# Performance work log

Hardware: AMD Instinct MI355X
Metric: run time of the kernel (lower is better)

Reference implementation:

```python
import jax, jax.numpy as jnp
import numpy as np
import math

FEAT_DIM = 128
N_BANK = 1000000
K_NEG = 4096
BATCH = 256
T = 0.5
MOMENTUM = 0.5
EPS = 1e-7


def setup_inputs() -> dict:
    key = jax.random.key(0)
    k1, k2, k3, k4, k5, k6 = jax.random.split(key, 6)
    stdv = 1.0 / math.sqrt(FEAT_DIM / 3)
    memory_l = jax.random.uniform(k1, (N_BANK, FEAT_DIM), minval=-stdv, maxval=stdv, dtype=jnp.float32)
    memory_ab = jax.random.uniform(k2, (N_BANK, FEAT_DIM), minval=-stdv, maxval=stdv, dtype=jnp.float32)
    l = jax.random.normal(k3, (BATCH, FEAT_DIM), dtype=jnp.float32)
    ab = jax.random.normal(k4, (BATCH, FEAT_DIM), dtype=jnp.float32)
    y = jax.random.randint(k5, (BATCH,), 0, N_BANK, dtype=jnp.int32)
    idx = jax.random.randint(k6, (BATCH, K_NEG + 1), 0, N_BANK, dtype=jnp.int32)
    idx = idx.at[:, 0].set(y)  # positive sample in slot 0, as in torch forward
    return {"l": l, "ab": ab, "memory_l": memory_l, "memory_ab": memory_ab, "y": y, "idx": idx}


def _l2_normalize(x):
    # matches torch: x / (sqrt(sum(x^2)) + eps)
    return x / (jnp.sqrt(jnp.sum(x * x, axis=1, keepdims=True)) + EPS)


def _momentum_update(memory, y, x_norm):
    # gather rows, momentum mix, renormalize, scatter back
    pos = memory[y] * MOMENTUM + x_norm * (1.0 - MOMENTUM)          # [B, D]
    norm = jnp.sqrt(jnp.sum(pos * pos, axis=1, keepdims=True))
    return memory.at[y].set(pos / norm)


def reference(l, ab, memory_l, memory_ab, y, idx):
    outputSize = memory_l.shape[0]
    ln = _l2_normalize(l)
    abn = _l2_normalize(ab)

    # gather negatives+positive from the AB bank, score against l features
    w_ab = jax.lax.stop_gradient(memory_ab[idx])                     # [B, K+1, D]
    P_l = jnp.exp(jnp.einsum('bkd,bd->bk', w_ab, ln) / T)[..., None]  # [B, K+1, 1]
    Z_l = jnp.mean(P_l) * outputSize
    out_l = P_l / Z_l

    w_l = jax.lax.stop_gradient(memory_l[idx])                       # [B, K+1, D]
    P_ab = jnp.exp(jnp.einsum('bkd,bd->bk', w_l, abn) / T)[..., None]
    Z_ab = jnp.mean(P_ab) * outputSize
    out_ab = P_ab / Z_ab

    # momentum scatter update of the memory banks (no_grad in torch)
    new_memory_l = jax.lax.stop_gradient(_momentum_update(memory_l, y, ln))
    new_memory_ab = jax.lax.stop_gradient(_momentum_update(memory_ab, y, abn))

    return out_l, out_ab, new_memory_l, new_memory_ab
```

## Files before the change

### kernel.cpp

```cpp
#include <hip/hip_runtime.h>
#include <math.h>
#include <stdint.h>

#define FEAT   128
#define NBANK  1000000
#define KP1    4097
#define BATCH  256
#define INV_T  2.0f
#define EPS_N  1e-7f

constexpr size_t TOTP   = (size_t)BATCH * KP1;
constexpr size_t O_OUTL = 0;
constexpr size_t O_OUTA = TOTP;
constexpr size_t O_MEML = 2 * TOTP;
constexpr size_t O_MEMA = O_MEML + (size_t)NBANK * FEAT;

constexpr int RPB   = 32;
constexpr int NBUCK = NBANK / RPB;

constexpr size_t WS_LN   = 0;
constexpr size_t WS_ABN  = 32768;
constexpr size_t WS_INVZ = 65536;
constexpr size_t WS_PL   = 65544;
constexpr size_t WS_PA   = 65800;
constexpr size_t WS_U32  = 66560;

typedef float vfloat4 __attribute__((ext_vector_type(4)));

__device__ __forceinline__ void nt_store4(vfloat4* p, vfloat4 v) {
    __builtin_nontemporal_store(v, p);
}
__device__ __forceinline__ float dot4(vfloat4 a, vfloat4 b) {
    return a.x * b.x + a.y * b.y + a.z * b.z + a.w * b.w;
}

__global__ void norm_kernel(const float* __restrict__ l,
                            const float* __restrict__ ab,
                            float* __restrict__ ws) {
    int b    = blockIdx.x;
    int lane = threadIdx.x;
    const float* src;
    float*       dst;
    if (b < BATCH) { src = l  + (size_t)b * FEAT;            dst = ws + WS_LN  + (size_t)b * FEAT; }
    else           { src = ab + (size_t)(b - BATCH) * FEAT;  dst = ws + WS_ABN + (size_t)(b - BATCH) * FEAT; }
    float2 v = *(const float2*)(src + 2 * lane);
    float  ss = v.x * v.x + v.y * v.y;
    #pragma unroll
    for (int m = 1; m < 64; m <<= 1) ss += __shfl_xor(ss, m, 64);
    float inv = 1.0f / (sqrtf(ss) + EPS_N);
    ((float2*)dst)[lane] = make_float2(v.x * inv, v.y * inv);
}

__global__ void zero_kernel(unsigned int* __restrict__ cnt) {
    int stride = gridDim.x * blockDim.x;
    for (int i = blockIdx.x * blockDim.x + threadIdx.x; i < NBUCK; i += stride)
        cnt[i] = 0u;
}

__global__ void hist_kernel(const int* __restrict__ idx,
                            unsigned int* __restrict__ cnt) {
    int stride = gridDim.x * blockDim.x;
    for (size_t p = (size_t)blockIdx.x * blockDim.x + threadIdx.x; p < TOTP; p += stride) {
        int row = idx[p];
        atomicAdd(&cnt[row >> 5], 1u);
    }
}

__global__ void scan_kernel(const unsigned int* __restrict__ cnt,
                            unsigned int* __restrict__ start,
                            unsigned int* __restrict__ cur) {
    __shared__ unsigned int ts[256];
    __shared__ unsigned int ex[256];
    int t = threadIdx.x;
    const int Q = (NBUCK + 255) / 256;
    int lo = t * Q, hi = lo + Q; if (hi > NBUCK) hi = NBUCK;
    unsigned int s = 0;
    for (int i = lo; i < hi; ++i) s += cnt[i];
    ts[t] = s;
    __syncthreads();
    if (t == 0) {
        unsigned int r = 0;
        for (int i = 0; i < 256; ++i) { ex[i] = r; r += ts[i]; }
    }
    __syncthreads();
    unsigned int base = ex[t];
    for (int i = lo; i < hi; ++i) {
        start[i] = base; cur[i] = base;
        base += cnt[i];
    }
}

__global__ void scatter_kernel(const int* __restrict__ idx,
                               unsigned int* __restrict__ cur,
                               unsigned int* __restrict__ ent) {
    int stride = gridDim.x * blockDim.x;
    for (size_t p = (size_t)blockIdx.x * blockDim.x + threadIdx.x; p < TOTP; p += stride) {
        int row = idx[p];
        int b   = (int)(p / KP1);
        int k   = (int)(p - (size_t)b * KP1);
        unsigned int pos = atomicAdd(&cur[row >> 5], 1u);
        ent[pos] = ((unsigned int)b << 18) | ((unsigned int)k << 5) | (unsigned int)(row & 31);
    }
}

__global__ __launch_bounds__(256) void main_kernel(
        const float* __restrict__ mem_l, const float* __restrict__ mem_ab,
        const float* __restrict__ ws_f,
        const unsigned int* __restrict__ start,
        const unsigned int* __restrict__ cur,
        const unsigned int* __restrict__ ent,
        float* __restrict__ out) {
    __shared__ float ldsL[RPB * FEAT];
    __shared__ float ldsA[RPB * FEAT];
    int blk = blockIdx.x;
    int tid = threadIdx.x;
    size_t fbase = (size_t)blk * RPB * FEAT;

    const vfloat4* sl = (const vfloat4*)(mem_l  + fbase);
    const vfloat4* sa = (const vfloat4*)(mem_ab + fbase);
    vfloat4* dl_ = (vfloat4*)(out + O_MEML + fbase);
    vfloat4* da_ = (vfloat4*)(out + O_MEMA + fbase);
    vfloat4* lL = (vfloat4*)ldsL;
    vfloat4* lA = (vfloat4*)ldsA;
    vfloat4 vl[4], va[4];
    #pragma unroll
    for (int j = 0; j < 4; ++j) { vl[j] = sl[j * 256 + tid]; }
    #pragma unroll
    for (int j = 0; j < 4; ++j) { va[j] = sa[j * 256 + tid]; }
    #pragma unroll
    for (int j = 0; j < 4; ++j) {
        int i = j * 256 + tid;
        lL[i] = vl[j]; nt_store4(dl_ + i, vl[j]);
        lA[i] = va[j]; nt_store4(da_ + i, va[j]);
    }
    __syncthreads();

    int s = (int)start[blk], e = (int)cur[blk];
    int g = tid >> 4, lane16 = tid & 15;
    for (int i = s + g; i < e; i += 16) {
        unsigned int ev = ent[i];
        int rloc = (int)(ev & 31u);
        int k    = (int)((ev >> 5) & 0x1FFFu);
        int b    = (int)(ev >> 18);
        const vfloat4* ra = (const vfloat4*)(ldsA + rloc * FEAT) + lane16 * 2;
        const vfloat4* rl = (const vfloat4*)(ldsL + rloc * FEAT) + lane16 * 2;
        vfloat4 wa0 = ra[0], wa1 = ra[1];
        vfloat4 wl0 = rl[0], wl1 = rl[1];
        const vfloat4* lq = (const vfloat4*)(ws_f + WS_LN  + (size_t)b * FEAT) + lane16 * 2;
        const vfloat4* aq = (const vfloat4*)(ws_f + WS_ABN + (size_t)b * FEAT) + lane16 * 2;
        vfloat4 lv0 = lq[0], lv1 = lq[1];
        vfloat4 av0 = aq[0], av1 = aq[1];
        float dl  = dot4(wa0, lv0) + dot4(wa1, lv1);
        float dab = dot4(wl0, av0) + dot4(wl1, av1);
        #pragma unroll
        for (int m = 1; m < 16; m <<= 1) {
            dl  += __shfl_xor(dl,  m, 64);
            dab += __shfl_xor(dab, m, 64);
        }
        if (lane16 == 0) {
            out[O_OUTL + (size_t)b * KP1 + k] = __expf(dl  * INV_T);
            out[O_OUTA + (size_t)b * KP1 + k] = __expf(dab * INV_T);
        }
    }
}

__global__ void zsum_kernel(const float* __restrict__ out,
                            float* __restrict__ pl, float* __restrict__ pa) {
    __shared__ float sl[256], sa[256];
    int i = blockIdx.x, t = threadIdx.x;
    const float* bl = out + O_OUTL + (size_t)i * KP1;
    const float* ba = out + O_OUTA + (size_t)i * KP1;
    float a = 0.f, b = 0.f;
    for (int p = t; p < KP1; p += 256) { a += bl[p]; b += ba[p]; }
    sl[t] = a; sa[t] = b;
    __syncthreads();
    for (int s = 128; s > 0; s >>= 1) {
        if (t < s) { sl[t] += sl[t + s]; sa[t] += sa[t + s]; }
        __syncthreads();
    }
    if (t == 0) { pl[i] = sl[0]; pa[i] = sa[0]; }
}

__global__ void zfinal_kernel(const float* __restrict__ pl,
                              const float* __restrict__ pa,
                              float* __restrict__ invz) {
    if (threadIdx.x == 0) {
        float a = 0.f, b = 0.f;
        for (int i = 0; i < 256; ++i) { a += pl[i]; b += pa[i]; }
        float count = (float)TOTP;
        invz[0] = count / (a * (float)NBANK);
        invz[1] = count / (b * (float)NBANK);
    }
}

__global__ void scale_kernel(float* __restrict__ out, const float* __restrict__ invz) {
    float zl = invz[0], za = invz[1];
    size_t stride = (size_t)gridDim.x * blockDim.x;
    for (size_t i = (size_t)blockIdx.x * blockDim.x + threadIdx.x; i < TOTP; i += stride) {
        out[O_OUTL + i] *= zl;
        out[O_OUTA + i] *= za;
    }
}

__global__ void update_kernel(const float* __restrict__ mem_l,
                              const float* __restrict__ mem_ab,
                              const int*   __restrict__ y,
                              const float* __restrict__ ws,
                              float* __restrict__ out) {
    int b    = blockIdx.x;
    int lane = threadIdx.x;
    int row  = y[b];
    for (int j = b + 1; j < BATCH; ++j)
        if (y[j] == row) return;
    {
        float2 m = ((const float2*)(mem_l + (size_t)row * FEAT))[lane];
        float2 x = ((const float2*)(ws + WS_LN + (size_t)b * FEAT))[lane];
        float2 p = make_float2(m.x * 0.5f + x.x * 0.5f, m.y * 0.5f + x.y * 0.5f);
        float ss = p.x * p.x + p.y * p.y;
        #pragma unroll
        for (int mk = 1; mk < 64; mk <<= 1) ss += __shfl_xor(ss, mk, 64);
        float nrm = sqrtf(ss);
        ((float2*)(out + O_MEML + (size_t)row * FEAT))[lane] =
            make_float2(p.x / nrm, p.y / nrm);
    }
    {
        float2 m = ((const float2*)(mem_ab + (size_t)row * FEAT))[lane];
        float2 x = ((const float2*)(ws + WS_ABN + (size_t)b * FEAT))[lane];
        float2 p = make_float2(m.x * 0.5f + x.x * 0.5f, m.y * 0.5f + x.y * 0.5f);
        float ss = p.x * p.x + p.y * p.y;
        #pragma unroll
        for (int mk = 1; mk < 64; mk <<= 1) ss += __shfl_xor(ss, mk, 64);
        float nrm = sqrtf(ss);
        ((float2*)(out + O_MEMA + (size_t)row * FEAT))[lane] =
            make_float2(p.x / nrm, p.y / nrm);
    }
}

extern "C" void kernel_launch(void* const* d_in, const int* in_sizes, int n_in,
                              void* d_out, int out_size, void* d_ws, size_t ws_size,
                              hipStream_t stream) {
    const float* l      = (const float*)d_in[0];
    const float* ab     = (const float*)d_in[1];
    const float* mem_l  = (const float*)d_in[2];
    const float* mem_ab = (const float*)d_in[3];
    const int*   y      = (const int*)d_in[4];
    const int*   idx    = (const int*)d_in[5];
    float* out = (float*)d_out;
    float* ws  = (float*)d_ws;

    unsigned int* wsu   = (unsigned int*)(ws + WS_U32);
    unsigned int* cnt   = wsu;
    unsigned int* start = wsu + NBUCK;
    unsigned int* cur   = wsu + 2 * (size_t)NBUCK;
    unsigned int* ent   = wsu + 3 * (size_t)NBUCK;

    norm_kernel<<<dim3(2 * BATCH), dim3(64), 0, stream>>>(l, ab, ws);
    zero_kernel   <<<dim3(128),  dim3(256), 0, stream>>>(cnt);
    hist_kernel   <<<dim3(2048), dim3(256), 0, stream>>>(idx, cnt);
    scan_kernel   <<<dim3(1),    dim3(256), 0, stream>>>(cnt, start, cur);
    scatter_kernel<<<dim3(2048), dim3(256), 0, stream>>>(idx, cur, ent);
    main_kernel<<<dim3(NBUCK), dim3(256), 0, stream>>>(
        mem_l, mem_ab, ws, start, cur, ent, out);
    zsum_kernel  <<<dim3(256), dim3(256), 0, stream>>>(out, ws + WS_PL, ws + WS_PA);
    zfinal_kernel<<<dim3(1),   dim3(64),  0, stream>>>(ws + WS_PL, ws + WS_PA, ws + WS_INVZ);
    scale_kernel<<<dim3(1024), dim3(256), 0, stream>>>(out, ws + WS_INVZ);
    update_kernel<<<dim3(BATCH), dim3(64), 0, stream>>>(mem_l, mem_ab, y, ws, out);
}
```

Measured before the change: 577.5 us.

## Replace histogram-scan bucketing with fixed-capacity per-bucket entry lists

Drops the separate zero, histogram, single-block scan and scatter passes. A single atomic pass now writes entries straight into fixed slots of up to 192 per 32-row bucket, and the counter zeroing is folded into the normalization kernel. The main kernel stages its bucket's entries in shared memory and uses ordinary stores instead of nontemporal stores for the bank copy. The intent is to cut kernel launches, the serial scan and one full pass over idx. Any bucket holding more than 192 entries would silently lose scores; with uniformly random indices that is very unlikely.

```diff
diff --git a/kernel.cpp b/kernel.cpp
--- a/kernel.cpp
+++ b/kernel.cpp
@@ -17,6 +17,7 @@
 
 constexpr int RPB   = 32;
 constexpr int NBUCK = NBANK / RPB;
+constexpr int CAP   = 192;
 
 constexpr size_t WS_LN   = 0;
 constexpr size_t WS_ABN  = 32768;
@@ -27,18 +28,18 @@
 
 typedef float vfloat4 __attribute__((ext_vector_type(4)));
 
-__device__ __forceinline__ void nt_store4(vfloat4* p, vfloat4 v) {
-    __builtin_nontemporal_store(v, p);
-}
 __device__ __forceinline__ float dot4(vfloat4 a, vfloat4 b) {
     return a.x * b.x + a.y * b.y + a.z * b.z + a.w * b.w;
 }
 
-__global__ void norm_kernel(const float* __restrict__ l,
-                            const float* __restrict__ ab,
-                            float* __restrict__ ws) {
+__global__ void norm_zero_kernel(const float* __restrict__ l,
+                                 const float* __restrict__ ab,
+                                 float* __restrict__ ws,
+                                 unsigned int* __restrict__ cnt) {
     int b    = blockIdx.x;
     int lane = threadIdx.x;
+    int gid  = b * 64 + lane;
+    if (gid < NBUCK) cnt[gid] = 0u;
     const float* src;
     float*       dst;
     if (b < BATCH) { src = l  + (size_t)b * FEAT;            dst = ws + WS_LN  + (size_t)b * FEAT; }
@@ -51,94 +52,60 @@
     ((float2*)dst)[lane] = make_float2(v.x * inv, v.y * inv);
 }
 
-__global__ void zero_kernel(unsigned int* __restrict__ cnt) {
-    int stride = gridDim.x * blockDim.x;
-    for (int i = blockIdx.x * blockDim.x + threadIdx.x; i < NBUCK; i += stride)
-        cnt[i] = 0u;
-}
-
-__global__ void hist_kernel(const int* __restrict__ idx,
-                            unsigned int* __restrict__ cnt) {
-    int stride = gridDim.x * blockDim.x;
-    for (size_t p = (size_t)blockIdx.x * blockDim.x + threadIdx.x; p < TOTP; p += stride) {
-        int row = idx[p];
-        atomicAdd(&cnt[row >> 5], 1u);
-    }
-}
-
-__global__ void scan_kernel(const unsigned int* __restrict__ cnt,
-                            unsigned int* __restrict__ start,
-                            unsigned int* __restrict__ cur) {
-    __shared__ unsigned int ts[256];
-    __shared__ unsigned int ex[256];
-    int t = threadIdx.x;
-    const int Q = (NBUCK + 255) / 256;
-    int lo = t * Q, hi = lo + Q; if (hi > NBUCK) hi = NBUCK;
-    unsigned int s = 0;
-    for (int i = lo; i < hi; ++i) s += cnt[i];
-    ts[t] = s;
-    __syncthreads();
-    if (t == 0) {
-        unsigned int r = 0;
-        for (int i = 0; i < 256; ++i) { ex[i] = r; r += ts[i]; }
-    }
-    __syncthreads();
-    unsigned int base = ex[t];
-    for (int i = lo; i < hi; ++i) {
-        start[i] = base; cur[i] = base;
-        base += cnt[i];
-    }
-}
-
-__global__ void scatter_kernel(const int* __restrict__ idx,
-                               unsigned int* __restrict__ cur,
-                               unsigned int* __restrict__ ent) {
-    int stride = gridDim.x * blockDim.x;
+__global__ void build_kernel(const int* __restrict__ idx,
+                             unsigned int* __restrict__ cnt,
+                             unsigned int* __restrict__ ent) {
+    size_t stride = (size_t)gridDim.x * blockDim.x;
     for (size_t p = (size_t)blockIdx.x * blockDim.x + threadIdx.x; p < TOTP; p += stride) {
         int row = idx[p];
         int b   = (int)(p / KP1);
         int k   = (int)(p - (size_t)b * KP1);
-        unsigned int pos = atomicAdd(&cur[row >> 5], 1u);
-        ent[pos] = ((unsigned int)b << 18) | ((unsigned int)k << 5) | (unsigned int)(row & 31);
+        int bucket = row >> 5;
+        unsigned int pos = atomicAdd(&cnt[bucket], 1u);
+        if (pos < (unsigned int)CAP)
+            ent[(size_t)bucket * CAP + pos] =
+                ((unsigned int)b << 18) | ((unsigned int)k << 5) | (unsigned int)(row & 31);
     }
 }
 
 __global__ __launch_bounds__(256) void main_kernel(
         const float* __restrict__ mem_l, const float* __restrict__ mem_ab,
         const float* __restrict__ ws_f,
-        const unsigned int* __restrict__ start,
-        const unsigned int* __restrict__ cur,
+        const unsigned int* __restrict__ cnt,
         const unsigned int* __restrict__ ent,
         float* __restrict__ out) {
     __shared__ float ldsL[RPB * FEAT];
     __shared__ float ldsA[RPB * FEAT];
+    __shared__ unsigned int sEnt[CAP];
     int blk = blockIdx.x;
     int tid = threadIdx.x;
     size_t fbase = (size_t)blk * RPB * FEAT;
 
     const vfloat4* sl = (const vfloat4*)(mem_l  + fbase);
     const vfloat4* sa = (const vfloat4*)(mem_ab + fbase);
+    vfloat4 vl[4], va[4];
+    #pragma unroll
+    for (int j = 0; j < 4; ++j) vl[j] = sl[j * 256 + tid];
+    #pragma unroll
+    for (int j = 0; j < 4; ++j) va[j] = sa[j * 256 + tid];
+
+    int c = min((int)cnt[blk], CAP);
+    for (int i = tid; i < c; i += 256) sEnt[i] = ent[(size_t)blk * CAP + i];
+
+    vfloat4* lL = (vfloat4*)ldsL;
+    vfloat4* lA = (vfloat4*)ldsA;
+    #pragma unroll
+    for (int j = 0; j < 4; ++j) { int i = j * 256 + tid; lL[i] = vl[j]; lA[i] = va[j]; }
+    __syncthreads();
+
     vfloat4* dl_ = (vfloat4*)(out + O_MEML + fbase);
     vfloat4* da_ = (vfloat4*)(out + O_MEMA + fbase);
-    vfloat4* lL = (vfloat4*)ldsL;
-    vfloat4* lA = (vfloat4*)ldsA;
-    vfloat4 vl[4], va[4];
-    #pragma unroll
-    for (int j = 0; j < 4; ++j) { vl[j] = sl[j * 256 + tid]; }
-    #pragma unroll
-    for (int j = 0; j < 4; ++j) { va[j] = sa[j * 256 + tid]; }
-    #pragma unroll
-    for (int j = 0; j < 4; ++j) {
-        int i = j * 256 + tid;
-        lL[i] = vl[j]; nt_store4(dl_ + i, vl[j]);
-        lA[i] = va[j]; nt_store4(da_ + i, va[j]);
-    }
-    __syncthreads();
-
-    int s = (int)start[blk], e = (int)cur[blk];
+    #pragma unroll
+    for (int j = 0; j < 4; ++j) { int i = j * 256 + tid; dl_[i] = vl[j]; da_[i] = va[j]; }
+
     int g = tid >> 4, lane16 = tid & 15;
-    for (int i = s + g; i < e; i += 16) {
-        unsigned int ev = ent[i];
+    for (int i = g; i < c; i += 16) {
+        unsigned int ev = sEnt[i];
         int rloc = (int)(ev & 31u);
         int k    = (int)((ev >> 5) & 0x1FFFu);
         int b    = (int)(ev >> 18);
@@ -248,19 +215,14 @@
     float* out = (float*)d_out;
     float* ws  = (float*)d_ws;
 
-    unsigned int* wsu   = (unsigned int*)(ws + WS_U32);
-    unsigned int* cnt   = wsu;
-    unsigned int* start = wsu + NBUCK;
-    unsigned int* cur   = wsu + 2 * (size_t)NBUCK;
-    unsigned int* ent   = wsu + 3 * (size_t)NBUCK;
-
-    norm_kernel<<<dim3(2 * BATCH), dim3(64), 0, stream>>>(l, ab, ws);
-    zero_kernel   <<<dim3(128),  dim3(256), 0, stream>>>(cnt);
-    hist_kernel   <<<dim3(2048), dim3(256), 0, stream>>>(idx, cnt);
-    scan_kernel   <<<dim3(1),    dim3(256), 0, stream>>>(cnt, start, cur);
-    scatter_kernel<<<dim3(2048), dim3(256), 0, stream>>>(idx, cur, ent);
+    unsigned int* wsu = (unsigned int*)(ws + WS_U32);
+    unsigned int* cnt = wsu;
+    unsigned int* ent = wsu + NBUCK;
+
+    norm_zero_kernel<<<dim3(2 * BATCH), dim3(64), 0, stream>>>(l, ab, ws, cnt);
+    build_kernel<<<dim3(2048), dim3(256), 0, stream>>>(idx, cnt, ent);
     main_kernel<<<dim3(NBUCK), dim3(256), 0, stream>>>(
-        mem_l, mem_ab, ws, start, cur, ent, out);
+        mem_l, mem_ab, ws, cnt, ent, out);
     zsum_kernel  <<<dim3(256), dim3(256), 0, stream>>>(out, ws + WS_PL, ws + WS_PA);
     zfinal_kernel<<<dim3(1),   dim3(64),  0, stream>>>(ws + WS_PL, ws + WS_PA, ws + WS_INVZ);
     scale_kernel<<<dim3(1024), dim3(256), 0, stream>>>(out, ws + WS_INVZ);
```

Result: faster. 490.9 us (-15.0%).
